# Kernel tuning notes

Hardware: AMD Instinct MI355X
Metric: run time of the kernel (lower is better)

Reference implementation:

```python
import jax, jax.numpy as jnp
import numpy as np

BT = 64  # time chunk size (matches Triton BT)


def _chunk_simple_gla(q, k, v, g):
    """Chunked simple-GLA / RWKV6c forward.
    q,k: [B,H,T,K]; v: [B,H,T,V]; g: [B,H,T] per-token log decay.
    Token-level math: S_t = exp(g_t)*S_{t-1} + k_t v_t^T ; o_t = scale * q_t @ S_t.
    Computed chunk-wise exactly as the Triton kernels do.
    """
    B, H, T, K = q.shape
    V = v.shape[-1]
    NT = T // BT
    scale = K ** -0.5

    qc = q.reshape(B, H, NT, BT, K)
    kc = k.reshape(B, H, NT, BT, K)
    vc = v.reshape(B, H, NT, BT, V)
    gc = jnp.cumsum(g.reshape(B, H, NT, BT), axis=-1)  # chunk-local cumulative log decay
    g_last = gc[..., -1]                               # [B,H,NT]

    # per-chunk kv contribution: sum_s k_s (v_s * exp(g_last - g_s))^T
    w = jnp.exp(g_last[..., None] - gc)                # [B,H,NT,BT]
    chunk_kv = jnp.einsum('bhntk,bhntv->bhnkv', kc, vc * w[..., None])
    decay = jnp.exp(g_last)                            # [B,H,NT]

    # inter-chunk state recurrence: h_n = state BEFORE chunk n
    def scan_fn(S, x):
        d, kv = x
        S_new = d[..., None, None] * S + kv
        return S_new, S  # emit state entering this chunk

    xs = (jnp.moveaxis(decay, 2, 0), jnp.moveaxis(chunk_kv, 2, 0))
    S0 = jnp.zeros((B, H, K, V), dtype=q.dtype)
    _, h = jax.lax.scan(scan_fn, S0, xs)               # h: [NT,B,H,K,V]
    h = jnp.moveaxis(h, 0, 2)                          # [B,H,NT,K,V]

    # inter-chunk output: exp(g_t) * q_t @ h_chunk * scale
    o_inter = jnp.einsum('bhntk,bhnkv->bhntv', qc, h) * jnp.exp(gc)[..., None] * scale

    # intra-chunk causal output with gated mask exp(g_i - g_j), i >= j
    s = jnp.einsum('bhnik,bhnjk->bhnij', qc, kc)
    mask = jnp.tril(jnp.ones((BT, BT), dtype=bool))
    s = jnp.where(mask, s * jnp.exp(gc[..., :, None] - gc[..., None, :]) * scale, 0.0)
    o_intra = jnp.einsum('bhnij,bhnjv->bhniv', s, vc)

    return (o_inter + o_intra).reshape(B, H, T, V)


def setup_inputs() -> dict:
    key = jax.random.key(0)
    kq, kk, kv, kg = jax.random.split(key, 4)
    B, H, T, K, V = 2, 32, 4096, 128, 128
    q = jax.random.normal(kq, (B, H, T, K), dtype=jnp.float32)
    k = jax.random.normal(kk, (B, H, T, K), dtype=jnp.float32)
    v = jax.random.normal(kv, (B, H, T, V), dtype=jnp.float32)
    # log-decay gates: negative so exp(cumsum) is bounded (RWKV6/GLA semantics)
    g = -0.5 * jax.random.uniform(kg, (B, H, T), dtype=jnp.float32)
    return {"q": q, "k": k, "v": v, "g": g}


def reference(q, k, v, g):
    return _chunk_simple_gla(q, k, v, g)
```

## Files before the change

kernel.cpp:

```cpp
#include <hip/hip_runtime.h>
#include <hip/hip_bf16.h>


#define BT 64
#define KD 128
#define VD 128
#define VSG 32
#define NCHUNK 64
#define TLEN 4096
#define SCALE 0.08838834764831845f

#define QSTR 136
#define SHSTR 72
#define SVSTR 136
#define VTSTR 72

typedef __bf16 bf16;
typedef __bf16 bf16x8 __attribute__((ext_vector_type(8)));
typedef __bf16 bf16x4 __attribute__((ext_vector_type(4)));
typedef float f32x4 __attribute__((ext_vector_type(4)));

#define MFMA __builtin_amdgcn_mfma_f32_16x16x32_bf16
#define LGKM_BARRIER() do { asm volatile("s_waitcnt lgkmcnt(0)" ::: "memory"); \
                            __builtin_amdgcn_s_barrier(); } while (0)

__device__ __forceinline__ int ksw(int t) { return ((t >> 3) & 3) << 5; }

__device__ __forceinline__ int vt_off(int vc, int t) {
  int byte = vc * (VTSTR * 2) + t * 2;
  byte ^= ((vc >> 2) & 7) << 4;
  return byte >> 1;
}

__device__ __forceinline__ bf16x8 frag_row(const bf16* p, int stride, int row0,
                                           int kk0, int lane) {
  int row = row0 + (lane & 15);
  int kk = kk0 + ((lane >> 4) << 3);
  return *(const bf16x8*)(p + row * stride + kk);
}

__device__ __forceinline__ bf16x8 krow_frag(const bf16* ks_, int row0, int kk0,
                                            int lane) {
  int row = row0 + (lane & 15);
  int kk = kk0 + ((lane >> 4) << 3);
  int byte = (row * (QSTR * 2) + kk * 2) ^ ksw(row);
  return *(const bf16x8*)((const char*)ks_ + byte);
}

__device__ __forceinline__ bf16x8 kcol_frag(const bf16* ks_, int T0, int kdA) {
  int C = ((T0 >> 3) & 3) << 5;
  int b0 = T0 * (QSTR * 2) + kdA * 2;
  bf16x8 f;
#pragma unroll
  for (int j = 0; j < 8; ++j)
    f[j] = *(const bf16*)((const char*)ks_ + ((b0 + j * (QSTR * 2)) ^ C));
  return f;
}

__device__ __forceinline__ void st4(bf16* p, float a, float b, float c, float d) {
  bf16x4 t;
  t[0] = (bf16)a; t[1] = (bf16)b; t[2] = (bf16)c; t[3] = (bf16)d;
  *(bf16x4*)p = t;
}

__global__ void __launch_bounds__(512, 2)
gla_fused(const float* __restrict__ qg, const float* __restrict__ kg,
          const float* __restrict__ vg, const float* __restrict__ gg,
          float* __restrict__ og)
{
  __shared__ __align__(16) bf16 q_s[BT * QSTR];
  __shared__ __align__(16) bf16 k_s[BT * QSTR];
  __shared__ __align__(16) bf16 vT_s[2][VSG * VTSTR];
  __shared__ __align__(16) bf16 vwT_s[2][VSG * VTSTR];
  __shared__ __align__(16) bf16 sh_s[BT * SHSTR];
  __shared__ __align__(16) bf16 svt_s[VSG * SVSTR];
  __shared__ __align__(16) float gc_all[NCHUNK][BT];
  __shared__ float glast_all[NCHUNK];

  const int tid = threadIdx.x;
  const int wave = tid >> 6;
  const int lane = tid & 63;
  const int bh = blockIdx.x & 63;
  const int vseg = blockIdx.x >> 6;

  const int jc = lane & 15;
  const int g4 = lane >> 4;
  const int r0 = g4 << 2;

  const int it = wave & 3;
  const int nt = wave >> 2;
  const int jt0 = (wave < 4) ? 0 : 2;

  const size_t qkbase = (size_t)bh * TLEN * KD;
  const size_t gbase = (size_t)bh * TLEN;
  const size_t vbase = (size_t)bh * TLEN * VD + (size_t)vseg * VSG;
  const int vrow = tid >> 3;
  const int vc0 = (tid & 7) << 2;

  float4 qpf[4], kpf[4], vpf;

  auto loadpf = [&](int n) {
    const float4* q4 = (const float4*)(qg + qkbase + (size_t)n * (BT * KD));
    const float4* k4 = (const float4*)(kg + qkbase + (size_t)n * (BT * KD));
#pragma unroll
    for (int i = 0; i < 4; ++i) { qpf[i] = q4[i * 512 + tid]; kpf[i] = k4[i * 512 + tid]; }
    vpf = *(const float4*)(vg + vbase + (size_t)(n * BT + vrow) * VD + vc0);
  };

  auto stage = [&](int buf, int n) {
#pragma unroll
    for (int i = 0; i < 4; ++i) {
      int f4 = i * 512 + tid;
      int t = f4 >> 5;
      int kd0 = (f4 & 31) << 2;
      st4(&q_s[t * QSTR + kd0], qpf[i].x, qpf[i].y, qpf[i].z, qpf[i].w);
      int byte = (t * (QSTR * 2) + kd0 * 2) ^ ksw(t);
      st4((bf16*)((char*)k_s + byte), kpf[i].x, kpf[i].y, kpf[i].z, kpf[i].w);
    }
    bf16* vt = &vT_s[buf][0];
    bf16* vwt = &vwT_s[buf][0];
    float wv = __expf(glast_all[n] - gc_all[n][vrow]);
    vt[vt_off(vc0 + 0, vrow)] = (bf16)vpf.x;
    vt[vt_off(vc0 + 1, vrow)] = (bf16)vpf.y;
    vt[vt_off(vc0 + 2, vrow)] = (bf16)vpf.z;
    vt[vt_off(vc0 + 3, vrow)] = (bf16)vpf.w;
    vwt[vt_off(vc0 + 0, vrow)] = (bf16)(vpf.x * wv);
    vwt[vt_off(vc0 + 1, vrow)] = (bf16)(vpf.y * wv);
    vwt[vt_off(vc0 + 2, vrow)] = (bf16)(vpf.z * wv);
    vwt[vt_off(vc0 + 3, vrow)] = (bf16)(vpf.w * wv);
  };

  f32x4 Sa = {0.f, 0.f, 0.f, 0.f}, Sb = {0.f, 0.f, 0.f, 0.f};

  loadpf(0);
#pragma unroll 1
  for (int i = 0; i < 8; ++i) {
    int cn = wave * 8 + i;
    float a = gg[gbase + cn * BT + lane];
#pragma unroll
    for (int off = 1; off < 64; off <<= 1) {
      float t = __shfl_up(a, off);
      if (lane >= off) a += t;
    }
    gc_all[cn][lane] = a;
    if (lane == 63) glast_all[cn] = a;
  }
  LGKM_BARRIER();
  stage(0, 0);
  LGKM_BARRIER();

  for (int n = 0; n < NCHUNK; ++n) {
    const int cur = n & 1;

    if (n + 1 < NCHUNK) loadpf(n + 1);

    bf16x8 af[4];
#pragma unroll
    for (int ks = 0; ks < 4; ++ks)
      af[ks] = frag_row(q_s, QSTR, it * 16, ks * 32, lane);

    st4(&svt_s[jc * SVSTR + wave * 16 + r0], Sa[0], Sa[1], Sa[2], Sa[3]);
    st4(&svt_s[(16 + jc) * SVSTR + wave * 16 + r0], Sb[0], Sb[1], Sb[2], Sb[3]);

    f32x4 sa0 = {0.f,0.f,0.f,0.f}, sa1 = {0.f,0.f,0.f,0.f};
#pragma unroll
    for (int ks = 0; ks < 4; ++ks) {
      bf16x8 a0 = krow_frag(k_s, jt0 * 16, ks * 32, lane);
      bf16x8 a1 = krow_frag(k_s, (jt0 + 1) * 16, ks * 32, lane);
      sa0 = MFMA(a0, af[ks], sa0, 0, 0, 0);
      sa1 = MFMA(a1, af[ks], sa1, 0, 0, 0);
    }
    {
      int i0 = it * 16 + jc;
      float gci = gc_all[n][i0];
#pragma unroll
      for (int t = 0; t < 2; ++t) {
        f32x4 sv = t ? sa1 : sa0;
        int jb = (jt0 + t) * 16 + r0;
        float4 g4v = *(const float4*)&gc_all[n][jb];
        const float* gj = (const float*)&g4v;
        bf16x4 pk;
#pragma unroll
        for (int r = 0; r < 4; ++r) {
          float val = (i0 >= jb + r) ? sv[r] * __expf(gci - gj[r]) * SCALE : 0.f;
          pk[r] = (bf16)val;
        }
        *(bf16x4*)&sh_s[i0 * SHSTR + jb] = pk;
      }
    }
    {
      float dec = __expf(glast_all[n]);
#pragma unroll
      for (int r = 0; r < 4; ++r) { Sa[r] *= dec; Sb[r] *= dec; }
#pragma unroll
      for (int ks = 0; ks < 2; ++ks) {
        bf16x8 a = kcol_frag(k_s, ks * 32 + (g4 << 3), wave * 16 + jc);
        bf16x8 b0 = *(const bf16x8*)(&vwT_s[cur][0] + vt_off(jc, ks * 32 + (g4 << 3)));
        bf16x8 b1 = *(const bf16x8*)(&vwT_s[cur][0] + vt_off(16 + jc, ks * 32 + (g4 << 3)));
        Sa = MFMA(a, b0, Sa, 0, 0, 0);
        Sb = MFMA(a, b1, Sb, 0, 0, 0);
      }
    }
    LGKM_BARRIER();

    {
      f32x4 oacc = {0.f, 0.f, 0.f, 0.f};
#pragma unroll
      for (int ks = 0; ks < 4; ++ks) {
        bf16x8 b = frag_row(svt_s, SVSTR, nt * 16, ks * 32, lane);
        oacc = MFMA(af[ks], b, oacc, 0, 0, 0);
      }
      {
        float4 e4 = *(const float4*)&gc_all[n][it * 16 + r0];
        const float* ep = (const float*)&e4;
#pragma unroll
        for (int r = 0; r < 4; ++r) oacc[r] *= __expf(ep[r]) * SCALE;
      }
#pragma unroll
      for (int ks = 0; ks < 2; ++ks) {
        bf16x8 a = frag_row(sh_s, SHSTR, it * 16, ks * 32, lane);
        bf16x8 b = *(const bf16x8*)(&vT_s[cur][0] + vt_off(nt * 16 + jc, ks * 32 + (g4 << 3)));
        oacc = MFMA(a, b, oacc, 0, 0, 0);
      }
#pragma unroll
      for (int r = 0; r < 4; ++r) {
        int row = it * 16 + r0 + r;
        og[vbase + (size_t)(n * BT + row) * VD + nt * 16 + jc] = oacc[r];
      }
    }
    if (n + 1 < NCHUNK) stage((n + 1) & 1, n + 1);
    LGKM_BARRIER();
  }
}

extern "C" void kernel_launch(void* const* d_in, const int* in_sizes, int n_in,
                              void* d_out, int out_size, void* d_ws, size_t ws_size,
                              hipStream_t stream) {
  const float* q = (const float*)d_in[0];
  const float* k = (const float*)d_in[1];
  const float* v = (const float*)d_in[2];
  const float* g = (const float*)d_in[3];
  float* o = (float*)d_out;
  dim3 grid(256);
  dim3 block(512);
  gla_fused<<<grid, block, 0, stream>>>(q, k, v, g, o);
}
```

Measured before the change: 186.0 us.

## Software-pipeline chunk loop: defer output emission and drop one barrier per chunk

Each chunk's output computation is moved into the next iteration, so only one LDS barrier per chunk is needed instead of two. To make this safe, the q/k, score and state-snapshot buffers are double-buffered and the v buffers triple-buffered. Global loads are prefetched two chunks ahead instead of one, giving more latency hiding. The cost is much higher LDS use, about 150KB, which rules out two blocks per CU; with a 256-block grid that may not matter. It also adds register pressure from holding the previous chunk's q fragments.

```diff
diff --git a/kernel.cpp b/kernel.cpp
--- a/kernel.cpp
+++ b/kernel.cpp
@@ -68,12 +68,12 @@
           const float* __restrict__ vg, const float* __restrict__ gg,
           float* __restrict__ og)
 {
-  __shared__ __align__(16) bf16 q_s[BT * QSTR];
-  __shared__ __align__(16) bf16 k_s[BT * QSTR];
-  __shared__ __align__(16) bf16 vT_s[2][VSG * VTSTR];
-  __shared__ __align__(16) bf16 vwT_s[2][VSG * VTSTR];
-  __shared__ __align__(16) bf16 sh_s[BT * SHSTR];
-  __shared__ __align__(16) bf16 svt_s[VSG * SVSTR];
+  __shared__ __align__(16) bf16 q_s[2][BT * QSTR];
+  __shared__ __align__(16) bf16 k_s[2][BT * QSTR];
+  __shared__ __align__(16) bf16 vT_s[3][VSG * VTSTR];
+  __shared__ __align__(16) bf16 vwT_s[3][VSG * VTSTR];
+  __shared__ __align__(16) bf16 sh_s[2][BT * SHSTR];
+  __shared__ __align__(16) bf16 svt_s[2][VSG * SVSTR];
   __shared__ __align__(16) float gc_all[NCHUNK][BT];
   __shared__ float glast_all[NCHUNK];
 
@@ -107,18 +107,18 @@
     vpf = *(const float4*)(vg + vbase + (size_t)(n * BT + vrow) * VD + vc0);
   };
 
-  auto stage = [&](int buf, int n) {
+  auto stage = [&](int b2, int b3, int n) {
 #pragma unroll
     for (int i = 0; i < 4; ++i) {
       int f4 = i * 512 + tid;
       int t = f4 >> 5;
       int kd0 = (f4 & 31) << 2;
-      st4(&q_s[t * QSTR + kd0], qpf[i].x, qpf[i].y, qpf[i].z, qpf[i].w);
+      st4(&q_s[b2][t * QSTR + kd0], qpf[i].x, qpf[i].y, qpf[i].z, qpf[i].w);
       int byte = (t * (QSTR * 2) + kd0 * 2) ^ ksw(t);
-      st4((bf16*)((char*)k_s + byte), kpf[i].x, kpf[i].y, kpf[i].z, kpf[i].w);
-    }
-    bf16* vt = &vT_s[buf][0];
-    bf16* vwt = &vwT_s[buf][0];
+      st4((bf16*)((char*)k_s[b2] + byte), kpf[i].x, kpf[i].y, kpf[i].z, kpf[i].w);
+    }
+    bf16* vt = vT_s[b3];
+    bf16* vwt = vwT_s[b3];
     float wv = __expf(glast_all[n] - gc_all[n][vrow]);
     vt[vt_off(vc0 + 0, vrow)] = (bf16)vpf.x;
     vt[vt_off(vc0 + 1, vrow)] = (bf16)vpf.y;
@@ -130,7 +130,34 @@
     vwt[vt_off(vc0 + 3, vrow)] = (bf16)(vpf.w * wv);
   };
 
+  auto o_emit = [&](int no, int b2o, int b3o, const bf16x8 (&afp)[4]) {
+    f32x4 oacc = {0.f, 0.f, 0.f, 0.f};
+#pragma unroll
+    for (int ks = 0; ks < 4; ++ks) {
+      bf16x8 b = frag_row(svt_s[b2o], SVSTR, nt * 16, ks * 32, lane);
+      oacc = MFMA(afp[ks], b, oacc, 0, 0, 0);
+    }
+    {
+      float4 e4 = *(const float4*)&gc_all[no][it * 16 + r0];
+      const float* ep = (const float*)&e4;
+#pragma unroll
+      for (int r = 0; r < 4; ++r) oacc[r] *= __expf(ep[r]) * SCALE;
+    }
+#pragma unroll
+    for (int ks = 0; ks < 2; ++ks) {
+      bf16x8 a = frag_row(sh_s[b2o], SHSTR, it * 16, ks * 32, lane);
+      bf16x8 b = *(const bf16x8*)(vT_s[b3o] + vt_off(nt * 16 + jc, ks * 32 + (g4 << 3)));
+      oacc = MFMA(a, b, oacc, 0, 0, 0);
+    }
+#pragma unroll
+    for (int r = 0; r < 4; ++r) {
+      int row = it * 16 + r0 + r;
+      og[vbase + (size_t)(no * BT + row) * VD + nt * 16 + jc] = oacc[r];
+    }
+  };
+
   f32x4 Sa = {0.f, 0.f, 0.f, 0.f}, Sb = {0.f, 0.f, 0.f, 0.f};
+  bf16x8 afp[4];
 
   loadpf(0);
 #pragma unroll 1
@@ -146,27 +173,29 @@
     if (lane == 63) glast_all[cn] = a;
   }
   LGKM_BARRIER();
-  stage(0, 0);
+  stage(0, 0, 0);
+  loadpf(1);
   LGKM_BARRIER();
 
+  int b3 = 0;
+#pragma unroll 1
   for (int n = 0; n < NCHUNK; ++n) {
-    const int cur = n & 1;
-
-    if (n + 1 < NCHUNK) loadpf(n + 1);
+    const int b2 = n & 1;
+    const int b3n = (b3 == 2) ? 0 : b3 + 1;
+    const int b3p = (b3 == 0) ? 2 : b3 - 1;
+
+    if (n > 0) o_emit(n - 1, b2 ^ 1, b3p, afp);
 
     bf16x8 af[4];
 #pragma unroll
     for (int ks = 0; ks < 4; ++ks)
-      af[ks] = frag_row(q_s, QSTR, it * 16, ks * 32, lane);
-
-    st4(&svt_s[jc * SVSTR + wave * 16 + r0], Sa[0], Sa[1], Sa[2], Sa[3]);
-    st4(&svt_s[(16 + jc) * SVSTR + wave * 16 + r0], Sb[0], Sb[1], Sb[2], Sb[3]);
+      af[ks] = frag_row(q_s[b2], QSTR, it * 16, ks * 32, lane);
 
     f32x4 sa0 = {0.f,0.f,0.f,0.f}, sa1 = {0.f,0.f,0.f,0.f};
 #pragma unroll
     for (int ks = 0; ks < 4; ++ks) {
-      bf16x8 a0 = krow_frag(k_s, jt0 * 16, ks * 32, lane);
-      bf16x8 a1 = krow_frag(k_s, (jt0 + 1) * 16, ks * 32, lane);
+      bf16x8 a0 = krow_frag(k_s[b2], jt0 * 16, ks * 32, lane);
+      bf16x8 a1 = krow_frag(k_s[b2], (jt0 + 1) * 16, ks * 32, lane);
       sa0 = MFMA(a0, af[ks], sa0, 0, 0, 0);
       sa1 = MFMA(a1, af[ks], sa1, 0, 0, 0);
     }
@@ -185,52 +214,39 @@
           float val = (i0 >= jb + r) ? sv[r] * __expf(gci - gj[r]) * SCALE : 0.f;
           pk[r] = (bf16)val;
         }
-        *(bf16x4*)&sh_s[i0 * SHSTR + jb] = pk;
+        *(bf16x4*)&sh_s[b2][i0 * SHSTR + jb] = pk;
       }
     }
+
+    st4(&svt_s[b2][jc * SVSTR + wave * 16 + r0], Sa[0], Sa[1], Sa[2], Sa[3]);
+    st4(&svt_s[b2][(16 + jc) * SVSTR + wave * 16 + r0], Sb[0], Sb[1], Sb[2], Sb[3]);
     {
       float dec = __expf(glast_all[n]);
 #pragma unroll
       for (int r = 0; r < 4; ++r) { Sa[r] *= dec; Sb[r] *= dec; }
 #pragma unroll
       for (int ks = 0; ks < 2; ++ks) {
-        bf16x8 a = kcol_frag(k_s, ks * 32 + (g4 << 3), wave * 16 + jc);
-        bf16x8 b0 = *(const bf16x8*)(&vwT_s[cur][0] + vt_off(jc, ks * 32 + (g4 << 3)));
-        bf16x8 b1 = *(const bf16x8*)(&vwT_s[cur][0] + vt_off(16 + jc, ks * 32 + (g4 << 3)));
+        bf16x8 a = kcol_frag(k_s[b2], ks * 32 + (g4 << 3), wave * 16 + jc);
+        bf16x8 b0 = *(const bf16x8*)(vwT_s[b3] + vt_off(jc, ks * 32 + (g4 << 3)));
+        bf16x8 b1 = *(const bf16x8*)(vwT_s[b3] + vt_off(16 + jc, ks * 32 + (g4 << 3)));
         Sa = MFMA(a, b0, Sa, 0, 0, 0);
         Sb = MFMA(a, b1, Sb, 0, 0, 0);
       }
     }
-    LGKM_BARRIER();
-
-    {
-      f32x4 oacc = {0.f, 0.f, 0.f, 0.f};
-#pragma unroll
-      for (int ks = 0; ks < 4; ++ks) {
-        bf16x8 b = frag_row(svt_s, SVSTR, nt * 16, ks * 32, lane);
-        oacc = MFMA(af[ks], b, oacc, 0, 0, 0);
-      }
-      {
-        float4 e4 = *(const float4*)&gc_all[n][it * 16 + r0];
-        const float* ep = (const float*)&e4;
-#pragma unroll
-        for (int r = 0; r < 4; ++r) oacc[r] *= __expf(ep[r]) * SCALE;
-      }
-#pragma unroll
-      for (int ks = 0; ks < 2; ++ks) {
-        bf16x8 a = frag_row(sh_s, SHSTR, it * 16, ks * 32, lane);
-        bf16x8 b = *(const bf16x8*)(&vT_s[cur][0] + vt_off(nt * 16 + jc, ks * 32 + (g4 << 3)));
-        oacc = MFMA(a, b, oacc, 0, 0, 0);
-      }
-#pragma unroll
-      for (int r = 0; r < 4; ++r) {
-        int row = it * 16 + r0 + r;
-        og[vbase + (size_t)(n * BT + row) * VD + nt * 16 + jc] = oacc[r];
-      }
-    }
-    if (n + 1 < NCHUNK) stage((n + 1) & 1, n + 1);
+
+    if (n + 1 < NCHUNK) {
+      stage(b2 ^ 1, b3n, n + 1);
+      if (n + 2 < NCHUNK) loadpf(n + 2);
+    }
+
+#pragma unroll
+    for (int ks = 0; ks < 4; ++ks) afp[ks] = af[ks];
+    b3 = b3n;
+
     LGKM_BARRIER();
   }
+
+  o_emit(NCHUNK - 1, 1, 0, afp);
 }
 
 extern "C" void kernel_launch(void* const* d_in, const int* in_sizes, int n_in,
```

New measurement: 161.9 us. 1.15x faster.
